# Kernel tuning notes

Hardware: AMD Instinct MI355X
Metric: run time of the kernel (lower is better)

## Reference

```python
import jax, jax.numpy as jnp
import numpy as np
import math

INPUT_SIZE = 128
HIDDEN_SIZE = 64
MEM_DIM = 64
B, S = 8, 2048


def _xavier(key, shape):
    fan_in, fan_out = shape[0], shape[1]
    a = math.sqrt(6.0 / (fan_in + fan_out))
    return jax.random.uniform(key, shape, jnp.float32, minval=-a, maxval=a)


def setup_inputs() -> dict:
    key = jax.random.key(0)
    ks = jax.random.split(key, 8)
    x = jax.random.normal(ks[0], (B, S, INPUT_SIZE), jnp.float32)
    return {
        "x": x,
        "c_prev": jnp.zeros((MEM_DIM, MEM_DIM), jnp.float32),
        "n_prev": jnp.zeros((MEM_DIM, 1), jnp.float32),
        "w_q": _xavier(ks[1], (INPUT_SIZE, HIDDEN_SIZE)),
        "b_q": jnp.zeros((HIDDEN_SIZE,), jnp.float32),
        "w_k": _xavier(ks[2], (INPUT_SIZE, MEM_DIM)),
        "b_k": jnp.zeros((MEM_DIM,), jnp.float32),
        "w_v": _xavier(ks[3], (INPUT_SIZE, MEM_DIM)),
        "b_v": jnp.zeros((MEM_DIM,), jnp.float32),
        "w_i": _xavier(ks[4], (INPUT_SIZE, 1)),
        "b_i": jnp.zeros((1,), jnp.float32),
        "w_f": _xavier(ks[5], (INPUT_SIZE, 1)),
        "b_f": jnp.zeros((1,), jnp.float32),
        "w_o": _xavier(ks[6], (INPUT_SIZE, HIDDEN_SIZE)),
        "b_o": jnp.zeros((HIDDEN_SIZE,), jnp.float32),
    }


def reference(x, c_prev, n_prev, w_q, b_q, w_k, b_k, w_v, b_v,
              w_i, b_i, w_f, b_f, w_o, b_o):
    b, s, d = x.shape
    mem_dim = w_k.shape[1]
    xf = x.reshape(b * s, d)  # [T, D], T = B*S

    q_t = xf @ w_q + b_q                                   # [T, H]
    k_t = (xf @ w_k + b_k) * (1.0 / math.sqrt(mem_dim))    # [T, M]
    v_t = xf @ w_v + b_v                                   # [T, M]
    i_t = jnp.exp(xf @ w_i + b_i)                          # [T, 1]
    f_t = jax.nn.sigmoid(xf @ w_f + b_f)                   # [T, 1]

    # Faithful to source: c_prev / n_prev are NEVER updated in the loop,
    # so every step mixes the same initial state -> fully parallel.
    # c_t[t] = f[t] * c_prev + i[t] * outer(v[t], k[t])
    c_t = (f_t[:, :, None] * c_prev[None]
           + i_t[:, :, None] * v_t[:, :, None] * k_t[:, None, :])  # [T, M, M]
    # n_t[t] = f[t] * n_prev + i[t] * k[t][:, None]
    n_t = f_t[:, :, None] * n_prev[None] + i_t[:, :, None] * k_t[:, :, None]  # [T, M, 1]

    c_t = c_t.reshape(b, s, mem_dim, mem_dim)
    n_t = n_t.reshape(b, s, mem_dim, 1)
    qv = q_t.reshape(b, s, mem_dim)  # requires hidden_size == mem_dim

    nq = jnp.einsum("bsm,bsm->bs", n_t[..., 0], qv)
    max_nqt = jnp.maximum(jnp.abs(nq), 1.0)                # [B, S]
    h_tilde = jnp.einsum("bsmk,bsk->bsm", c_t, qv) / max_nqt[..., None]

    o_t = jax.nn.sigmoid(xf @ w_o + b_o).reshape(b, s, -1)
    h_t = o_t * h_tilde                                    # [B, S, H]
    return (h_t, c_t, n_t)
```

## Files before the change

kernel.cpp:

```cpp
#include <hip/hip_runtime.h>
#include <cstdint>

#define NTOK 16384

typedef float f4 __attribute__((ext_vector_type(4)));
typedef __attribute__((ext_vector_type(4))) float f32x4;
typedef __attribute__((ext_vector_type(8))) short bf16x8;

__device__ __forceinline__ float readlane_f(float v, int lane) {
  return __int_as_float(__builtin_amdgcn_readlane(__float_as_int(v), lane));
}

__device__ __forceinline__ float wave_sum64(float v) {
  #pragma unroll
  for (int s = 1; s < 64; s <<= 1) v += __shfl_xor(v, s, 64);
  return v;
}

__device__ __forceinline__ float half_sum32(float v) {
  #pragma unroll
  for (int s = 1; s < 32; s <<= 1) v += __shfl_xor(v, s, 64);
  return v;
}

__device__ __forceinline__ uint32_t rne_bf16(float f) {
  uint32_t u = __float_as_uint(f);
  return (u + 0x7FFFu + ((u >> 16) & 1u)) >> 16;
}

__global__ void __launch_bounds__(512, 2)
fused_kernel(const float* __restrict__ x,
             const float* __restrict__ c_prev,
             const float* __restrict__ n_prev,
             const float* __restrict__ w_q, const float* __restrict__ b_q,
             const float* __restrict__ w_k, const float* __restrict__ b_k,
             const float* __restrict__ w_v, const float* __restrict__ b_v,
             const float* __restrict__ w_i, const float* __restrict__ b_i,
             const float* __restrict__ w_f, const float* __restrict__ b_f,
             const float* __restrict__ w_o, const float* __restrict__ b_o,
             float* __restrict__ h_out,
             float* __restrict__ c_out,
             float* __restrict__ n_out)
{
  __shared__ uint32_t smem[16384];
  __shared__ float    cp[64][68];
  const int tid  = threadIdx.x;
  const int lane = tid & 63;
  const int wid  = tid >> 6;
  const int T0   = blockIdx.x * 64;

  {
    const int n   = tid & 255;
    const int col = n & 63;
    const float* W = (n < 128) ? ((n < 64) ? w_q : w_k)
                               : ((n < 192) ? w_v : w_o);
    const int kph = tid >> 8;
    #pragma unroll
    for (int it = 0; it < 32; ++it) {
      const int kp = it * 2 + kph;
      const float a = W[(2 * kp)     * 64 + col];
      const float b = W[(2 * kp + 1) * 64 + col];
      const uint32_t pk = rne_bf16(a) | (rne_bf16(b) << 16);
      const int unit = (n << 4) + ((kp >> 2) ^ (n & 15));
      smem[(unit << 2) + (kp & 3)] = pk;
    }
  }
  for (int idx = tid; idx < 4096; idx += 512)
    cp[idx >> 6][idx & 63] = c_prev[idx];

  const f4* xp = (const f4*)(x + (size_t)(T0 + wid * 8) * 128);
  f4 xc[4];
  xc[0] = xp[lane];
  xc[1] = xp[64 + lane];
  xc[2] = xp[128 + lane];
  xc[3] = xp[192 + lane];

  __syncthreads();

  const int mt  = wid & 3;
  const int ntg = (wid >> 2) * 8;
  bf16x8 afrag[4];
  {
    const float* xr = x + (size_t)(T0 + mt * 16 + (lane & 15)) * 128
                        + ((lane >> 4) * 8);
    #pragma unroll
    for (int ks = 0; ks < 4; ++ks) {
      const f4 lo = *(const f4*)(xr + ks * 32);
      const f4 hi = *(const f4*)(xr + ks * 32 + 4);
      union { uint32_t u[4]; bf16x8 v; } cv;
      cv.u[0] = rne_bf16(lo.x) | (rne_bf16(lo.y) << 16);
      cv.u[1] = rne_bf16(lo.z) | (rne_bf16(lo.w) << 16);
      cv.u[2] = rne_bf16(hi.x) | (rne_bf16(hi.y) << 16);
      cv.u[3] = rne_bf16(hi.z) | (rne_bf16(hi.w) << 16);
      afrag[ks] = cv.v;
    }
  }
  f32x4 acc[8];
  #pragma unroll
  for (int j = 0; j < 8; ++j) acc[j] = (f32x4){0.f, 0.f, 0.f, 0.f};
  {
    const int bsub = lane & 15, bh = lane >> 4;
    #pragma unroll
    for (int nti = 0; nti < 8; ++nti) {
      const int n = (ntg + nti) * 16 + bsub;
      #pragma unroll
      for (int ks = 0; ks < 4; ++ks) {
        const int unit = (n << 4) + ((ks * 4 + bh) ^ (n & 15));
        const bf16x8 bfrag = *(const bf16x8*)&smem[unit << 2];
        acc[nti] = __builtin_amdgcn_mfma_f32_16x16x32_bf16(afrag[ks], bfrag,
                                                           acc[nti], 0, 0, 0);
      }
    }
  }
  __syncthreads();
  {
    float* y = (float*)smem;
    const int trow = mt * 16 + (lane >> 4) * 4;
    const int fcol = lane & 15;
    #pragma unroll
    for (int nti = 0; nti < 8; ++nti) {
      const int f = (ntg + nti) * 16 + fcol;
      #pragma unroll
      for (int r = 0; r < 4; ++r)
        y[(trow + r) * 256 + f] = acc[nti][r];
    }
  }
  __syncthreads();

  float itv[8], ftv[8];
  {
    const int dbase = (lane & 31) << 2;
    const f4 wi4 = *(const f4*)&w_i[dbase];
    const f4 wf4 = *(const f4*)&w_f[dbase];
    const float sbi = b_i[0], sbf = b_f[0];
    #pragma unroll
    for (int c = 0; c < 4; ++c) {
      float pi = xc[c].x * wi4.x + xc[c].y * wi4.y + xc[c].z * wi4.z + xc[c].w * wi4.w;
      float pf = xc[c].x * wf4.x + xc[c].y * wf4.y + xc[c].z * wf4.z + xc[c].w * wf4.w;
      pi = half_sum32(pi);
      pf = half_sum32(pf);
      itv[2 * c]     = __expf(readlane_f(pi, 0)  + sbi);
      itv[2 * c + 1] = __expf(readlane_f(pi, 32) + sbi);
      ftv[2 * c]     = 1.0f / (1.0f + __expf(-(readlane_f(pf, 0)  + sbf)));
      ftv[2 * c + 1] = 1.0f / (1.0f + __expf(-(readlane_f(pf, 32) + sbf)));
    }
  }

  const float bq = b_q[lane], bk = b_k[lane], bv = b_v[lane], bo = b_o[lane];
  const float npv = n_prev[lane];
  const int   m   = lane & 15;
  const float* y  = (const float*)smem;

  #pragma unroll 1
  for (int tt = 0; tt < 8; ++tt) {
    const int    tl = wid * 8 + tt;
    const size_t t  = (size_t)(T0 + tl);
    const float q   = y[tl * 256 + lane] + bq;
    const float k   = (y[tl * 256 + 64 + lane] + bk) * 0.125f;
    const float v   = y[tl * 256 + 128 + lane] + bv;
    const float o   = 1.0f / (1.0f + __expf(-(y[tl * 256 + 192 + lane] + bo)));
    const float it_ = itv[tt];
    const float ft_ = ftv[tt];

    const float n_val = fmaf(ft_, npv, it_ * k);
    n_out[t * 64 + lane] = n_val;

    const float nq = wave_sum64(n_val * q);
    const float kq = wave_sum64(k * q);

    float c0 = 0.f, c1 = 0.f, c2 = 0.f, c3 = 0.f;
    #pragma unroll
    for (int j = 0; j < 16; ++j) {
      const f4 r4 = *(const f4*)&cp[lane][4 * j];
      c0 = fmaf(r4.x, readlane_f(q, 4 * j),     c0);
      c1 = fmaf(r4.y, readlane_f(q, 4 * j + 1), c1);
      c2 = fmaf(r4.z, readlane_f(q, 4 * j + 2), c2);
      c3 = fmaf(r4.w, readlane_f(q, 4 * j + 3), c3);
    }
    const float cpq = (c0 + c1) + (c2 + c3);

    const float inv  = 1.0f / fmaxf(fabsf(nq), 1.0f);
    const float htil = fmaf(ft_, cpq, it_ * v * kq) * inv;
    h_out[t * 64 + lane] = o * htil;

    const float iv = it_ * v;
    const float k40 = __shfl(k, 4 * m, 64);
    const float k41 = __shfl(k, 4 * m + 1, 64);
    const float k42 = __shfl(k, 4 * m + 2, 64);
    const float k43 = __shfl(k, 4 * m + 3, 64);
    f4* ct = (f4*)(c_out + t * 4096);
    #pragma unroll
    for (int s = 0; s < 16; ++s) {
      const int row = 4 * s + (lane >> 4);
      const float ivr = __shfl(iv, row, 64);
      const f4 c4 = *(const f4*)&cp[row][4 * m];
      f4 val;
      val.x = fmaf(ft_, c4.x, ivr * k40);
      val.y = fmaf(ft_, c4.y, ivr * k41);
      val.z = fmaf(ft_, c4.z, ivr * k42);
      val.w = fmaf(ft_, c4.w, ivr * k43);
      ct[s * 64 + lane] = val;
    }
  }
}

extern "C" void kernel_launch(void* const* d_in, const int* in_sizes, int n_in,
                              void* d_out, int out_size, void* d_ws, size_t ws_size,
                              hipStream_t stream) {
  const float* x      = (const float*)d_in[0];
  const float* c_prev = (const float*)d_in[1];
  const float* n_prev = (const float*)d_in[2];
  const float* w_q = (const float*)d_in[3];
  const float* b_q = (const float*)d_in[4];
  const float* w_k = (const float*)d_in[5];
  const float* b_k = (const float*)d_in[6];
  const float* w_v = (const float*)d_in[7];
  const float* b_v = (const float*)d_in[8];
  const float* w_i = (const float*)d_in[9];
  const float* b_i = (const float*)d_in[10];
  const float* w_f = (const float*)d_in[11];
  const float* b_f = (const float*)d_in[12];
  const float* w_o = (const float*)d_in[13];
  const float* b_o = (const float*)d_in[14];

  float* h_out = (float*)d_out;
  float* c_out = h_out + 1048576;
  float* n_out = c_out + 67108864;

  fused_kernel<<<256, 512, 0, stream>>>(x, c_prev, n_prev,
                                        w_q, b_q, w_k, b_k, w_v, b_v,
                                        w_i, b_i, w_f, b_f, w_o, b_o,
                                        h_out, c_out, n_out);
}
```

Before: 55.66 us.

## Halve tokens per block, split weight staging in two passes, store projections as bf16

Each block now handles 32 tokens instead of 64 and the grid doubles to 512 blocks. The weight matrices are staged in LDS in two halves (q/k, then v/o), reusing one smaller buffer, and the projection results are written to LDS as bf16 with a padded pitch. The goal is to cut shared memory per block so more blocks fit per CU (launch bounds raised to 4), giving better latency hiding for the store-bound c_out writes. In exchange, the weight conversion is repeated across twice as many blocks, there are extra barriers, and storing intermediates as bf16 loses precision.

Result: slower. 108.3 us (+94.5%).

```diff
diff --git a/kernel.cpp b/kernel.cpp
--- a/kernel.cpp
+++ b/kernel.cpp
@@ -2,6 +2,8 @@
 #include <cstdint>
 
 #define NTOK 16384
+#define TPB 32
+#define YPITCH 264
 
 typedef float f4 __attribute__((ext_vector_type(4)));
 typedef __attribute__((ext_vector_type(4))) float f32x4;
@@ -28,7 +30,11 @@
   return (u + 0x7FFFu + ((u >> 16) & 1u)) >> 16;
 }
 
-__global__ void __launch_bounds__(512, 2)
+__device__ __forceinline__ float bf16f(uint32_t u) {
+  return __uint_as_float(u << 16);
+}
+
+__global__ void __launch_bounds__(512, 4)
 fused_kernel(const float* __restrict__ x,
              const float* __restrict__ c_prev,
              const float* __restrict__ n_prev,
@@ -42,43 +48,36 @@
              float* __restrict__ c_out,
              float* __restrict__ n_out)
 {
-  __shared__ uint32_t smem[16384];
+  __shared__ uint32_t wbuf[8192];
   __shared__ float    cp[64][68];
   const int tid  = threadIdx.x;
   const int lane = tid & 63;
   const int wid  = tid >> 6;
-  const int T0   = blockIdx.x * 64;
-
-  {
-    const int n   = tid & 255;
+  const int T0   = blockIdx.x * TPB;
+
+  {
+    const int n   = tid & 127;
     const int col = n & 63;
-    const float* W = (n < 128) ? ((n < 64) ? w_q : w_k)
-                               : ((n < 192) ? w_v : w_o);
-    const int kph = tid >> 8;
-    #pragma unroll
-    for (int it = 0; it < 32; ++it) {
-      const int kp = it * 2 + kph;
-      const float a = W[(2 * kp)     * 64 + col];
-      const float b = W[(2 * kp + 1) * 64 + col];
-      const uint32_t pk = rne_bf16(a) | (rne_bf16(b) << 16);
+    const float* W = (n < 64) ? w_q : w_k;
+    const int kph = tid >> 7;
+    #pragma unroll
+    for (int it = 0; it < 16; ++it) {
+      const int kp = it * 4 + kph;
+      const uint32_t pk = rne_bf16(W[(2 * kp) * 64 + col])
+                        | (rne_bf16(W[(2 * kp + 1) * 64 + col]) << 16);
       const int unit = (n << 4) + ((kp >> 2) ^ (n & 15));
-      smem[(unit << 2) + (kp & 3)] = pk;
+      wbuf[(unit << 2) + (kp & 3)] = pk;
     }
   }
   for (int idx = tid; idx < 4096; idx += 512)
     cp[idx >> 6][idx & 63] = c_prev[idx];
 
-  const f4* xp = (const f4*)(x + (size_t)(T0 + wid * 8) * 128);
-  f4 xc[4];
+  const f4* xp = (const f4*)(x + (size_t)(T0 + wid * 4) * 128);
+  f4 xc[2];
   xc[0] = xp[lane];
   xc[1] = xp[64 + lane];
-  xc[2] = xp[128 + lane];
-  xc[3] = xp[192 + lane];
-
-  __syncthreads();
-
-  const int mt  = wid & 3;
-  const int ntg = (wid >> 2) * 8;
+
+  const int mt = wid & 1;
   bf16x8 afrag[4];
   {
     const float* xr = x + (size_t)(T0 + mt * 16 + (lane & 15)) * 128
@@ -95,46 +94,79 @@
       afrag[ks] = cv.v;
     }
   }
-  f32x4 acc[8];
-  #pragma unroll
-  for (int j = 0; j < 8; ++j) acc[j] = (f32x4){0.f, 0.f, 0.f, 0.f};
-  {
-    const int bsub = lane & 15, bh = lane >> 4;
-    #pragma unroll
-    for (int nti = 0; nti < 8; ++nti) {
-      const int n = (ntg + nti) * 16 + bsub;
+
+  __syncthreads();
+
+  const int ntg  = (wid >> 1) * 2;
+  const int bsub = lane & 15, bh = lane >> 4;
+  f32x4 acc_qk[2] = {(f32x4){0.f,0.f,0.f,0.f}, (f32x4){0.f,0.f,0.f,0.f}};
+  #pragma unroll
+  for (int nti = 0; nti < 2; ++nti) {
+    const int n = (ntg + nti) * 16 + bsub;
+    #pragma unroll
+    for (int ks = 0; ks < 4; ++ks) {
+      const int unit = (n << 4) + ((ks * 4 + bh) ^ (n & 15));
+      const bf16x8 bfrag = *(const bf16x8*)&wbuf[unit << 2];
+      acc_qk[nti] = __builtin_amdgcn_mfma_f32_16x16x32_bf16(afrag[ks], bfrag,
+                                                            acc_qk[nti], 0, 0, 0);
+    }
+  }
+  __syncthreads();
+
+  {
+    const int n   = tid & 127;
+    const int col = n & 63;
+    const float* W = (n < 64) ? w_v : w_o;
+    const int kph = tid >> 7;
+    #pragma unroll
+    for (int it = 0; it < 16; ++it) {
+      const int kp = it * 4 + kph;
+      const uint32_t pk = rne_bf16(W[(2 * kp) * 64 + col])
+                        | (rne_bf16(W[(2 * kp + 1) * 64 + col]) << 16);
+      const int unit = (n << 4) + ((kp >> 2) ^ (n & 15));
+      wbuf[(unit << 2) + (kp & 3)] = pk;
+    }
+  }
+  __syncthreads();
+
+  f32x4 acc_vo[2] = {(f32x4){0.f,0.f,0.f,0.f}, (f32x4){0.f,0.f,0.f,0.f}};
+  #pragma unroll
+  for (int nti = 0; nti < 2; ++nti) {
+    const int n = (ntg + nti) * 16 + bsub;
+    #pragma unroll
+    for (int ks = 0; ks < 4; ++ks) {
+      const int unit = (n << 4) + ((ks * 4 + bh) ^ (n & 15));
+      const bf16x8 bfrag = *(const bf16x8*)&wbuf[unit << 2];
+      acc_vo[nti] = __builtin_amdgcn_mfma_f32_16x16x32_bf16(afrag[ks], bfrag,
+                                                            acc_vo[nti], 0, 0, 0);
+    }
+  }
+  __syncthreads();
+
+  {
+    uint16_t* y16 = (uint16_t*)wbuf;
+    const int trow = mt * 16 + (lane >> 4) * 4;
+    const int fb   = ntg * 16;
+    #pragma unroll
+    for (int nti = 0; nti < 2; ++nti) {
+      const int f = fb + nti * 16 + bsub;
       #pragma unroll
-      for (int ks = 0; ks < 4; ++ks) {
-        const int unit = (n << 4) + ((ks * 4 + bh) ^ (n & 15));
-        const bf16x8 bfrag = *(const bf16x8*)&smem[unit << 2];
-        acc[nti] = __builtin_amdgcn_mfma_f32_16x16x32_bf16(afrag[ks], bfrag,
-                                                           acc[nti], 0, 0, 0);
+      for (int r = 0; r < 4; ++r) {
+        y16[(trow + r) * YPITCH + f]       = (uint16_t)rne_bf16(acc_qk[nti][r]);
+        y16[(trow + r) * YPITCH + 128 + f] = (uint16_t)rne_bf16(acc_vo[nti][r]);
       }
     }
   }
   __syncthreads();
-  {
-    float* y = (float*)smem;
-    const int trow = mt * 16 + (lane >> 4) * 4;
-    const int fcol = lane & 15;
-    #pragma unroll
-    for (int nti = 0; nti < 8; ++nti) {
-      const int f = (ntg + nti) * 16 + fcol;
-      #pragma unroll
-      for (int r = 0; r < 4; ++r)
-        y[(trow + r) * 256 + f] = acc[nti][r];
-    }
-  }
-  __syncthreads();
-
-  float itv[8], ftv[8];
+
+  float itv[4], ftv[4];
   {
     const int dbase = (lane & 31) << 2;
     const f4 wi4 = *(const f4*)&w_i[dbase];
     const f4 wf4 = *(const f4*)&w_f[dbase];
     const float sbi = b_i[0], sbf = b_f[0];
     #pragma unroll
-    for (int c = 0; c < 4; ++c) {
+    for (int c = 0; c < 2; ++c) {
       float pi = xc[c].x * wi4.x + xc[c].y * wi4.y + xc[c].z * wi4.z + xc[c].w * wi4.w;
       float pf = xc[c].x * wf4.x + xc[c].y * wf4.y + xc[c].z * wf4.z + xc[c].w * wf4.w;
       pi = half_sum32(pi);
@@ -149,16 +181,17 @@
   const float bq = b_q[lane], bk = b_k[lane], bv = b_v[lane], bo = b_o[lane];
   const float npv = n_prev[lane];
   const int   m   = lane & 15;
-  const float* y  = (const float*)smem;
+  const uint16_t* y16 = (const uint16_t*)wbuf;
 
   #pragma unroll 1
-  for (int tt = 0; tt < 8; ++tt) {
-    const int    tl = wid * 8 + tt;
+  for (int tt = 0; tt < 4; ++tt) {
+    const int    tl = wid * 4 + tt;
     const size_t t  = (size_t)(T0 + tl);
-    const float q   = y[tl * 256 + lane] + bq;
-    const float k   = (y[tl * 256 + 64 + lane] + bk) * 0.125f;
-    const float v   = y[tl * 256 + 128 + lane] + bv;
-    const float o   = 1.0f / (1.0f + __expf(-(y[tl * 256 + 192 + lane] + bo)));
+    const uint16_t* yt = y16 + tl * YPITCH;
+    const float q   = bf16f(yt[lane]) + bq;
+    const float k   = (bf16f(yt[64 + lane]) + bk) * 0.125f;
+    const float v   = bf16f(yt[128 + lane]) + bv;
+    const float o   = 1.0f / (1.0f + __expf(-(bf16f(yt[192 + lane]) + bo)));
     const float it_ = itv[tt];
     const float ft_ = ftv[tt];
 
@@ -227,7 +260,7 @@
   float* c_out = h_out + 1048576;
   float* n_out = c_out + 67108864;
 
-  fused_kernel<<<256, 512, 0, stream>>>(x, c_prev, n_prev,
+  fused_kernel<<<512, 512, 0, stream>>>(x, c_prev, n_prev,
                                         w_q, b_q, w_k, b_k, w_v, b_v,
                                         w_i, b_i, w_f, b_f, w_o, b_o,
                                         h_out, c_out, n_out);
```
